# Optimization experiments

Hardware: AMD Instinct MI355X
Metric: run time of the kernel (lower is better)

## Reference

```python
import jax, jax.numpy as jnp
import numpy as np

EPS = 1e-6  # RMSNorm eps


def rms_norm(x, w):
    var = jnp.mean(jnp.square(x), axis=-1, keepdims=True)
    return x * jax.lax.rsqrt(var + EPS) * w


def setup_inputs() -> dict:
    B, N, D, L = 16, 4096, 512, 64
    key = jax.random.key(0)
    ks = jax.random.split(key, 12)
    query = jax.random.normal(ks[0], (B, D), jnp.float32)
    tokens = jax.random.normal(ks[1], (B, N, D), jnp.float32)
    padding_mask = jax.random.bernoulli(ks[2], 0.3, (B, N))  # True = padded
    latents = jax.random.normal(ks[3], (L, D), jnp.float32) * 0.02
    s = D ** -0.5
    Wq = jax.random.uniform(ks[4], (D, D), jnp.float32, -s, s)
    bq = jax.random.uniform(ks[5], (D,), jnp.float32, -s, s)
    Wk = jax.random.uniform(ks[6], (D, D), jnp.float32, -s, s)
    bk = jax.random.uniform(ks[7], (D,), jnp.float32, -s, s)
    Wv = jax.random.uniform(ks[8], (D, D), jnp.float32, -s, s)
    bv = jax.random.uniform(ks[9], (D,), jnp.float32, -s, s)
    norm_w = jnp.ones((D,), jnp.float32)
    return {"query": query, "tokens": tokens, "padding_mask": padding_mask,
            "latents": latents, "Wq": Wq, "bq": bq, "Wk": Wk, "bk": bk,
            "Wv": Wv, "bv": bv, "norm_w": norm_w}


def reference(query, tokens, padding_mask, latents, Wq, bq, Wk, bk, Wv, bv, norm_w):
    D = query.shape[-1]
    L = latents.shape[0]
    score_scale = float(D) ** -0.5

    valid = (~padding_mask).astype(tokens.dtype)[..., None]          # [B,N,1]
    masked_tokens = tokens * valid                                    # [B,N,D]

    latent_query = latents[None] + (query @ Wq + bq)[:, None, :]      # [B,L,D]
    keys = masked_tokens @ Wk + bk                                    # [B,N,D]
    values = (masked_tokens @ Wv + bv) * valid                        # [B,N,D]

    scores = jnp.einsum('bld,bnd->bln', latent_query, keys) * score_scale
    all_padded = jnp.all(padding_mask, axis=1, keepdims=True)         # [B,1]
    # safe key padding mask: if a row is entirely padded, unmask it to keep softmax finite
    safe_mask = (padding_mask & ~all_padded)[:, None, :]              # [B,1,N]
    scores = jnp.where(safe_mask, jnp.finfo(scores.dtype).min, scores)
    weights = jax.nn.softmax(scores.astype(jnp.float32), axis=-1).astype(values.dtype)

    out = jnp.einsum('bln,bnd->bld', weights, values)                 # [B,L,D]
    out = rms_norm(out, norm_w)
    out = out * (~all_padded).astype(out.dtype)[..., None]
    latent_mask = jnp.broadcast_to(all_padded, (all_padded.shape[0], L))
    return out, latent_mask
```

## Files before the change

kernel.cpp:

```cpp
#include <hip/hip_runtime.h>
#include <hip/hip_bf16.h>
#include <math.h>

#define BB 16
#define NN_ 4096
#define DD 512
#define LL 64
#define SCALE 0.044194173824159216f
#define RMS_EPS 1e-6f
#define MASKVAL -3.0e38f
#define PSZ (BB * LL * DD)
#define ZCH 16

using bf16x8 = __attribute__((ext_vector_type(8))) short;
using f32x4  = __attribute__((ext_vector_type(4))) float;

__device__ __forceinline__ unsigned short f2bf(float x) {
    return __bfloat16_as_ushort(__float2bfloat16(x));
}

__global__ __launch_bounds__(256) void k_qproj(const float* __restrict__ query, const float* __restrict__ Wq,
                                               const float* __restrict__ bq, float* __restrict__ qproj) {
    const int b = blockIdx.y;
    const int dl = threadIdx.x & 63;
    const int d = (blockIdx.x << 6) + dl;
    const int wv = threadIdx.x >> 6;
    __shared__ float q[DD];
    __shared__ float red[4][64];
    for (int e = threadIdx.x; e < DD; e += 256) q[e] = query[b * DD + e];
    __syncthreads();
    float acc = 0.f;
    #pragma unroll 8
    for (int i = 0; i < 128; ++i) {
        const int e = (wv << 7) + i;
        acc += q[e] * Wq[(size_t)e * DD + d];
    }
    red[wv][dl] = acc;
    __syncthreads();
    if (threadIdx.x < 64) {
        const int dd = (blockIdx.x << 6) + threadIdx.x;
        qproj[(size_t)b * DD + dd] = red[0][threadIdx.x] + red[1][threadIdx.x] +
                                     red[2][threadIdx.x] + red[3][threadIdx.x] + bq[dd];
    }
}

__global__ __launch_bounds__(256) void k_lkqk(const float* __restrict__ latents, const float* __restrict__ qproj,
                                              const float* __restrict__ Wk, const float* __restrict__ bk,
                                              float* __restrict__ Lk, float* __restrict__ Qk,
                                              float* __restrict__ sbL, float* __restrict__ sbQ) {
    const int r = blockIdx.y;
    const int e0 = blockIdx.x << 6;
    const int tid = threadIdx.x;
    __shared__ float row[DD];
    const float* src = (r < LL) ? (latents + (size_t)r * DD) : (qproj + (size_t)(r - LL) * DD);
    for (int dd = tid; dd < DD; dd += 256) row[dd] = src[dd];
    __syncthreads();
    const int e = e0 + (tid >> 2);
    const int part = tid & 3;
    const float4* w4 = (const float4*)(Wk + (size_t)e * DD);
    const float4* r4 = (const float4*)row;
    float acc = 0.f;
    #pragma unroll 8
    for (int j = 0; j < 32; ++j) {
        const int d4 = part + (j << 2);
        const float4 w = w4[d4], rr = r4[d4];
        acc += w.x * rr.x + w.y * rr.y + w.z * rr.z + w.w * rr.w;
    }
    acc += __shfl_xor(acc, 1);
    acc += __shfl_xor(acc, 2);
    if (part == 0) {
        if (r < LL) Lk[(size_t)r * DD + e] = acc;
        else        Qk[(size_t)(r - LL) * DD + e] = acc;
    }
    if (blockIdx.x == 0 && tid < 64) {
        float p = 0.f;
        #pragma unroll
        for (int dd = tid; dd < DD; dd += 64) p += bk[dd] * row[dd];
        #pragma unroll
        for (int off = 32; off > 0; off >>= 1) p += __shfl_xor(p, off);
        if (tid == 0) { if (r < LL) sbL[r] = p; else sbQ[r - LL] = p; }
    }
}

__global__ __launch_bounds__(512, 2) void k_flash(const float* __restrict__ tokens,
                                                  const float* __restrict__ Lk, const float* __restrict__ Qk,
                                                  const float* __restrict__ sbL, const float* __restrict__ sbQ,
                                                  const int* __restrict__ pmask,
                                                  float* __restrict__ part,
                                                  float* __restrict__ mz, float* __restrict__ sz) {
    const int z = blockIdx.x, b = blockIdx.y;
    const int tid = threadIdx.x;
    const int lane = tid & 63, w = tid >> 6;
    const int r16 = lane & 15, kl = lane >> 4;

    __shared__ unsigned short sB[64][72];
    __shared__ int sTdn[512][36];
    __shared__ unsigned short sP[64][72];
    __shared__ float sS[64][68];
    __shared__ float smem_m[64], smem_s[64], smem_rr[64], smem_ps[64];

    const int lq = (w & 3) << 4;
    const int nq = (w >> 2) << 5;
    bf16x8 afLQ[16];
    {
        const int l = lq + r16;
        #pragma unroll
        for (int f = 0; f < 16; ++f) {
            const int kb = (f << 5) + (kl << 3);
            const float4 a0 = *(const float4*)&Lk[(size_t)l * DD + kb];
            const float4 a1 = *(const float4*)&Lk[(size_t)l * DD + kb + 4];
            const float4 q0 = *(const float4*)&Qk[(size_t)b * DD + kb];
            const float4 q1 = *(const float4*)&Qk[(size_t)b * DD + kb + 4];
            bf16x8 v;
            v[0] = (short)f2bf(a0.x + q0.x); v[1] = (short)f2bf(a0.y + q0.y);
            v[2] = (short)f2bf(a0.z + q0.z); v[3] = (short)f2bf(a0.w + q0.w);
            v[4] = (short)f2bf(a1.x + q1.x); v[5] = (short)f2bf(a1.y + q1.y);
            v[6] = (short)f2bf(a1.z + q1.z); v[7] = (short)f2bf(a1.w + q1.w);
            afLQ[f] = v;
        }
    }

    f32x4 acc[4][4];
    #pragma unroll
    for (int m = 0; m < 4; ++m)
        #pragma unroll
        for (int ef = 0; ef < 4; ++ef)
            acc[m][ef] = (f32x4){0.f, 0.f, 0.f, 0.f};

    if (tid < 64) { smem_m[tid] = MASKVAL; smem_s[tid] = 0.f; }
    __syncthreads();

    const float sq = sbQ[b];
    const int n2 = tid >> 4;
    const int d4 = (tid & 15) << 2;

    for (int t4 = 0; t4 < 4; ++t4) {
        const int n0 = (z << 8) + (t4 << 6);
        f32x4 accS[2];
        accS[0] = (f32x4){0.f, 0.f, 0.f, 0.f};
        accS[1] = (f32x4){0.f, 0.f, 0.f, 0.f};

        float4 ra, rc;
        {
            const float* p0 = &tokens[(size_t)((b << 12) + n0 + (n2 << 1)) * DD + d4];
            ra = *(const float4*)p0; rc = *(const float4*)(p0 + DD);
        }
        #pragma unroll
        for (int s8 = 0; s8 < 8; ++s8) {
            const int d0 = s8 << 6;
            {
                ushort4 oa, oc;
                oa.x = f2bf(ra.x); oa.y = f2bf(ra.y); oa.z = f2bf(ra.z); oa.w = f2bf(ra.w);
                oc.x = f2bf(rc.x); oc.y = f2bf(rc.y); oc.z = f2bf(rc.z); oc.w = f2bf(rc.w);
                *(ushort4*)&sB[(n2 << 1)][d4] = oa;
                *(ushort4*)&sB[(n2 << 1) + 1][d4] = oc;
                const float* ap = (const float*)&ra;
                const float* cp = (const float*)&rc;
                #pragma unroll
                for (int j = 0; j < 4; ++j) {
                    const int drow = d0 + d4 + j;
                    const int phys = n2 ^ (((drow >> 2) & 7) << 2);
                    sTdn[drow][phys] = (int)((unsigned)f2bf(ap[j]) | ((unsigned)f2bf(cp[j]) << 16));
                }
            }
            __syncthreads();
            if (s8 < 7) {
                const float* p1 = &tokens[(size_t)((b << 12) + n0 + (n2 << 1)) * DD + ((s8 + 1) << 6) + d4];
                ra = *(const float4*)p1; rc = *(const float4*)(p1 + DD);
            }
            #pragma unroll
            for (int kk2 = 0; kk2 < 2; ++kk2) {
                const int f = (s8 << 1) + kk2;
                #pragma unroll
                for (int nf = 0; nf < 2; ++nf) {
                    const bf16x8 bfr = *(const bf16x8*)&sB[nq + (nf << 4) + r16][(kk2 << 5) + (kl << 3)];
                    accS[nf] = __builtin_amdgcn_mfma_f32_16x16x32_bf16(afLQ[f], bfr, accS[nf], 0, 0, 0);
                }
            }
            __syncthreads();
        }

        #pragma unroll
        for (int nf = 0; nf < 2; ++nf) {
            const int ncol = nq + (nf << 4) + r16;
            const int pm = pmask[(size_t)b * NN_ + n0 + ncol];
            #pragma unroll
            for (int q = 0; q < 4; ++q) {
                const int l = lq + (kl << 2) + q;
                const float sval = (accS[nf][q] + sbL[l] + sq) * SCALE;
                sS[l][ncol] = pm ? MASKVAL : sval;
            }
        }
        __syncthreads();

        const int lrow = tid >> 3, j8 = (tid & 7) << 3;
        float4 v0 = *(const float4*)&sS[lrow][j8];
        float4 v1 = *(const float4*)&sS[lrow][j8 + 4];
        float tm = fmaxf(fmaxf(fmaxf(v0.x, v0.y), fmaxf(v0.z, v0.w)),
                         fmaxf(fmaxf(v1.x, v1.y), fmaxf(v1.z, v1.w)));
        tm = fmaxf(tm, __shfl_xor(tm, 1));
        tm = fmaxf(tm, __shfl_xor(tm, 2));
        tm = fmaxf(tm, __shfl_xor(tm, 4));
        float ex[8];
        ex[0] = __expf(v0.x - tm); ex[1] = __expf(v0.y - tm);
        ex[2] = __expf(v0.z - tm); ex[3] = __expf(v0.w - tm);
        ex[4] = __expf(v1.x - tm); ex[5] = __expf(v1.y - tm);
        ex[6] = __expf(v1.z - tm); ex[7] = __expf(v1.w - tm);
        float ts = ex[0] + ex[1] + ex[2] + ex[3] + ex[4] + ex[5] + ex[6] + ex[7];
        ts += __shfl_xor(ts, 1);
        ts += __shfl_xor(ts, 2);
        ts += __shfl_xor(ts, 4);
        if ((tid & 7) == 0) {
            const float mo = smem_m[lrow];
            const float mn = fmaxf(mo, tm);
            const float rrr = __expf(mo - mn);
            const float psc = __expf(tm - mn);
            smem_m[lrow] = mn;
            smem_s[lrow] = smem_s[lrow] * rrr + ts * psc;
            smem_rr[lrow] = rrr;
            smem_ps[lrow] = psc;
        }
        __syncthreads();

        {
            const float psc = smem_ps[lrow];
            bf16x8 pv;
            pv[0] = (short)f2bf(ex[0] * psc); pv[1] = (short)f2bf(ex[1] * psc);
            pv[2] = (short)f2bf(ex[2] * psc); pv[3] = (short)f2bf(ex[3] * psc);
            pv[4] = (short)f2bf(ex[4] * psc); pv[5] = (short)f2bf(ex[5] * psc);
            pv[6] = (short)f2bf(ex[6] * psc); pv[7] = (short)f2bf(ex[7] * psc);
            *(bf16x8*)&sP[lrow][j8] = pv;
        }
        #pragma unroll
        for (int m = 0; m < 4; ++m) {
            #pragma unroll
            for (int q = 0; q < 4; ++q) {
                const float rrr = smem_rr[(m << 4) + (kl << 2) + q];
                #pragma unroll
                for (int ef = 0; ef < 4; ++ef) acc[m][ef][q] *= rrr;
            }
        }
        __syncthreads();

        #pragma unroll
        for (int kk = 0; kk < 2; ++kk) {
            bf16x8 pa[4];
            #pragma unroll
            for (int m = 0; m < 4; ++m)
                pa[m] = *(const bf16x8*)&sP[(m << 4) + r16][(kk << 5) + (kl << 3)];
            #pragma unroll
            for (int ef = 0; ef < 4; ++ef) {
                const int e = (w << 6) + (ef << 4) + r16;
                const int g = (kk << 4) + (kl << 2);
                const int phys = g ^ (((e >> 2) & 7) << 2);
                const bf16x8 bv = *(const bf16x8*)&sTdn[e][phys];
                #pragma unroll
                for (int m = 0; m < 4; ++m)
                    acc[m][ef] = __builtin_amdgcn_mfma_f32_16x16x32_bf16(pa[m], bv, acc[m][ef], 0, 0, 0);
            }
        }
        __syncthreads();
    }

    #pragma unroll
    for (int m = 0; m < 4; ++m) {
        #pragma unroll
        for (int ef = 0; ef < 4; ++ef) {
            #pragma unroll
            for (int q = 0; q < 4; ++q) {
                const int l = (m << 4) + (kl << 2) + q;
                const int e = (w << 6) + (ef << 4) + r16;
                part[(size_t)((z << 10) + (b << 6) + l) * DD + e] = acc[m][ef][q];
            }
        }
    }
    if (tid < 64) {
        mz[(z << 10) + (b << 6) + tid] = smem_m[tid];
        sz[(z << 10) + (b << 6) + tid] = smem_s[tid];
    }
}

__global__ __launch_bounds__(256) void k_combine(const float* __restrict__ part,
                                                 const float* __restrict__ mz, const float* __restrict__ sz,
                                                 float* __restrict__ pacc, float* __restrict__ dmg) {
    const int row = blockIdx.x;
    const int t = threadIdx.x;
    float mv[ZCH];
    float mg = MASKVAL;
    #pragma unroll
    for (int zz = 0; zz < ZCH; ++zz) {
        mv[zz] = mz[(zz << 10) + row];
        mg = fmaxf(mg, mv[zz]);
    }
    float fz[ZCH];
    float den = 0.f;
    #pragma unroll
    for (int zz = 0; zz < ZCH; ++zz) {
        fz[zz] = __expf(mv[zz] - mg);
        den += sz[(zz << 10) + row] * fz[zz];
    }
    float a0 = 0.f, a1 = 0.f;
    #pragma unroll
    for (int zz = 0; zz < ZCH; ++zz) {
        const size_t base = (size_t)((zz << 10) + row) * DD;
        a0 += part[base + t] * fz[zz];
        a1 += part[base + t + 256] * fz[zz];
    }
    const float inv = 1.f / den;
    pacc[(size_t)row * DD + t] = a0 * inv;
    pacc[(size_t)row * DD + t + 256] = a1 * inv;
    if (t == 0) dmg[row] = mg;
}

__global__ __launch_bounds__(256) void k_proj(const float* __restrict__ pacc, const float* __restrict__ Wv,
                                              const float* __restrict__ bv, float* __restrict__ proj) {
    const int d0 = blockIdx.x * 64;
    const int r0 = blockIdx.y * 64;
    const int tid = threadIdx.x;
    const int rsub = (tid >> 4) << 2;
    const int dsub = (tid & 15) << 2;
    __shared__ float at[64][68];
    __shared__ float wv[64][68];
    float acc[4][4] = {{0.f, 0.f, 0.f, 0.f}};
    for (int kc = 0; kc < 8; ++kc) {
        const int k0 = kc * 64;
        for (int k = tid; k < 1024; k += 256) {
            const int rr = k >> 4, c4 = (k & 15) << 2;
            *(float4*)&at[rr][c4] = *(const float4*)&pacc[(size_t)(r0 + rr) * DD + k0 + c4];
            *(float4*)&wv[rr][c4] = *(const float4*)&Wv[(size_t)(k0 + rr) * DD + d0 + c4];
        }
        __syncthreads();
        #pragma unroll
        for (int n4 = 0; n4 < 16; ++n4) {
            float4 a4[4];
            #pragma unroll
            for (int i = 0; i < 4; ++i) a4[i] = *(const float4*)&at[rsub + i][n4 << 2];
            const float4 b0 = *(const float4*)&wv[(n4 << 2) + 0][dsub];
            const float4 b1 = *(const float4*)&wv[(n4 << 2) + 1][dsub];
            const float4 b2 = *(const float4*)&wv[(n4 << 2) + 2][dsub];
            const float4 b3 = *(const float4*)&wv[(n4 << 2) + 3][dsub];
            #pragma unroll
            for (int i = 0; i < 4; ++i) {
                const float4 av = a4[i];
                acc[i][0] += av.x * b0.x + av.y * b1.x + av.z * b2.x + av.w * b3.x;
                acc[i][1] += av.x * b0.y + av.y * b1.y + av.z * b2.y + av.w * b3.y;
                acc[i][2] += av.x * b0.z + av.y * b1.z + av.z * b2.z + av.w * b3.z;
                acc[i][3] += av.x * b0.w + av.y * b1.w + av.z * b2.w + av.w * b3.w;
            }
        }
        __syncthreads();
    }
    #pragma unroll
    for (int i = 0; i < 4; ++i) {
        const int d = d0 + dsub;
        float4 v;
        v.x = acc[i][0] + bv[d + 0];
        v.y = acc[i][1] + bv[d + 1];
        v.z = acc[i][2] + bv[d + 2];
        v.w = acc[i][3] + bv[d + 3];
        *(float4*)&proj[(size_t)(r0 + rsub + i) * DD + d] = v;
    }
}

__global__ __launch_bounds__(256) void k_rmsout(const float* __restrict__ proj, const float* __restrict__ norm_w,
                                                const float* __restrict__ dmg, float* __restrict__ out) {
    const int row = blockIdx.x;
    const int tid = threadIdx.x;
    __shared__ float red[256];
    const float* pr = proj + (size_t)row * DD;
    const float v0 = pr[tid], v1 = pr[tid + 256];
    red[tid] = v0 * v0 + v1 * v1;
    __syncthreads();
    for (int st = 128; st > 0; st >>= 1) {
        if (tid < st) red[tid] += red[tid + st];
        __syncthreads();
    }
    const float var = red[0] / (float)DD;
    const float r = 1.0f / sqrtf(var + RMS_EPS);
    const int ap = (dmg[row] < -1.0e38f) ? 1 : 0;
    const float msk = ap ? 0.f : 1.f;
    out[(size_t)row * DD + tid]       = v0 * r * norm_w[tid] * msk;
    out[(size_t)row * DD + tid + 256] = v1 * r * norm_w[tid + 256] * msk;
    if (tid == 0) out[(size_t)PSZ + row] = ap ? 1.f : 0.f;
}

extern "C" void kernel_launch(void* const* d_in, const int* in_sizes, int n_in,
                              void* d_out, int out_size, void* d_ws, size_t ws_size,
                              hipStream_t stream) {
    const float* query   = (const float*)d_in[0];
    const float* tokens  = (const float*)d_in[1];
    const int*   pmask   = (const int*)d_in[2];
    const float* latents = (const float*)d_in[3];
    const float* Wq = (const float*)d_in[4];
    const float* bq = (const float*)d_in[5];
    const float* Wk = (const float*)d_in[6];
    const float* bk = (const float*)d_in[7];
    const float* Wv = (const float*)d_in[8];
    const float* bv = (const float*)d_in[9];
    const float* nw = (const float*)d_in[10];

    float* ws = (float*)d_ws;
    float* dmg    = ws;
    float* mzv    = ws + 1024;
    float* szv    = ws + 17408;
    float* qproj  = ws + 33792;
    float* Lk     = ws + 41984;
    float* Qk     = ws + 74752;
    float* sbL    = ws + 82944;
    float* sbQ    = ws + 83008;
    float* part   = ws + 83072;
    float* pacc   = ws + 83072 + 8388608;
    float* proj   = ws + 83072 + 8388608 + 524288;
    float* out    = (float*)d_out;

    k_qproj<<<dim3(8, 16), 256, 0, stream>>>(query, Wq, bq, qproj);
    k_lkqk<<<dim3(8, 80), 256, 0, stream>>>(latents, qproj, Wk, bk, Lk, Qk, sbL, sbQ);
    k_flash<<<dim3(ZCH, 16), 512, 0, stream>>>(tokens, Lk, Qk, sbL, sbQ, pmask, part, mzv, szv);
    k_combine<<<1024, 256, 0, stream>>>(part, mzv, szv, pacc, dmg);
    k_proj<<<dim3(8, 16), 256, 0, stream>>>(pacc, Wv, bv, proj);
    k_rmsout<<<1024, 256, 0, stream>>>(proj, nw, dmg, out);
}
```

Measured before the change: 105.0 us.

## Shrink flash LDS footprint, double split-K chunks, store partials in fp16

The token split is doubled from 16 to 32 chunks, so each block handles 128 tokens, and the occupancy hint rises from 2 to 6 blocks per CU. LDS is cut by dropping the large transposed token tile; tokens are re-read from global per wave into a small per-wave swizzled tile for the PV matmul. Softmax now works on register scores with cross-wave max/sum reductions instead of an LDS score matrix. Partial outputs are stored in fp16 to halve combine traffic, at some cost in precision and extra global token reads.

```diff
diff --git a/kernel.cpp b/kernel.cpp
--- a/kernel.cpp
+++ b/kernel.cpp
@@ -10,7 +10,7 @@
 #define RMS_EPS 1e-6f
 #define MASKVAL -3.0e38f
 #define PSZ (BB * LL * DD)
-#define ZCH 16
+#define ZCH 32
 
 using bf16x8 = __attribute__((ext_vector_type(8))) short;
 using f32x4  = __attribute__((ext_vector_type(4))) float;
@@ -82,22 +82,22 @@
     }
 }
 
-__global__ __launch_bounds__(512, 2) void k_flash(const float* __restrict__ tokens,
+__global__ __launch_bounds__(512, 6) void k_flash(const float* __restrict__ tokens,
                                                   const float* __restrict__ Lk, const float* __restrict__ Qk,
                                                   const float* __restrict__ sbL, const float* __restrict__ sbQ,
                                                   const int* __restrict__ pmask,
-                                                  float* __restrict__ part,
+                                                  _Float16* __restrict__ part,
                                                   float* __restrict__ mz, float* __restrict__ sz) {
     const int z = blockIdx.x, b = blockIdx.y;
     const int tid = threadIdx.x;
     const int lane = tid & 63, w = tid >> 6;
     const int r16 = lane & 15, kl = lane >> 4;
 
-    __shared__ unsigned short sB[64][72];
-    __shared__ int sTdn[512][36];
+    __shared__ int sB[64][32];
     __shared__ unsigned short sP[64][72];
-    __shared__ float sS[64][68];
-    __shared__ float smem_m[64], smem_s[64], smem_rr[64], smem_ps[64];
+    __shared__ int sT[8][64][16];
+    __shared__ float s_mn[64], s_sum[64], s_rr[64];
+    __shared__ float s_pmax[2][64], s_psum[2][64];
 
     const int lq = (w & 3) << 4;
     const int nq = (w >> 2) << 5;
@@ -120,6 +120,11 @@
         }
     }
 
+    float sbl[4];
+    #pragma unroll
+    for (int q = 0; q < 4; ++q) sbl[q] = sbL[lq + (kl << 2) + q];
+    const float sq = sbQ[b];
+
     f32x4 acc[4][4];
     #pragma unroll
     for (int m = 0; m < 4; ++m)
@@ -127,15 +132,17 @@
         for (int ef = 0; ef < 4; ++ef)
             acc[m][ef] = (f32x4){0.f, 0.f, 0.f, 0.f};
 
-    if (tid < 64) { smem_m[tid] = MASKVAL; smem_s[tid] = 0.f; }
+    if (tid < 64) { s_mn[tid] = MASKVAL; s_sum[tid] = 0.f; }
     __syncthreads();
 
-    const float sq = sbQ[b];
     const int n2 = tid >> 4;
-    const int d4 = (tid & 15) << 2;
-
-    for (int t4 = 0; t4 < 4; ++t4) {
-        const int n0 = (z << 8) + (t4 << 6);
+    const int l15 = tid & 15;
+    const int d4 = l15 << 2;
+    const int gB = (((n2 << 1) >> 2) & 7) << 2;
+    const int phB = ((l15 << 1) ^ gB);
+
+    for (int t = 0; t < 2; ++t) {
+        const int n0 = (z << 7) + (t << 6);
         f32x4 accS[2];
         accS[0] = (f32x4){0.f, 0.f, 0.f, 0.f};
         accS[1] = (f32x4){0.f, 0.f, 0.f, 0.f};
@@ -147,21 +154,14 @@
         }
         #pragma unroll
         for (int s8 = 0; s8 < 8; ++s8) {
-            const int d0 = s8 << 6;
             {
-                ushort4 oa, oc;
-                oa.x = f2bf(ra.x); oa.y = f2bf(ra.y); oa.z = f2bf(ra.z); oa.w = f2bf(ra.w);
-                oc.x = f2bf(rc.x); oc.y = f2bf(rc.y); oc.z = f2bf(rc.z); oc.w = f2bf(rc.w);
-                *(ushort4*)&sB[(n2 << 1)][d4] = oa;
-                *(ushort4*)&sB[(n2 << 1) + 1][d4] = oc;
-                const float* ap = (const float*)&ra;
-                const float* cp = (const float*)&rc;
-                #pragma unroll
-                for (int j = 0; j < 4; ++j) {
-                    const int drow = d0 + d4 + j;
-                    const int phys = n2 ^ (((drow >> 2) & 7) << 2);
-                    sTdn[drow][phys] = (int)((unsigned)f2bf(ap[j]) | ((unsigned)f2bf(cp[j]) << 16));
-                }
+                int2 wa, wc;
+                wa.x = (int)((unsigned)f2bf(ra.x) | ((unsigned)f2bf(ra.y) << 16));
+                wa.y = (int)((unsigned)f2bf(ra.z) | ((unsigned)f2bf(ra.w) << 16));
+                wc.x = (int)((unsigned)f2bf(rc.x) | ((unsigned)f2bf(rc.y) << 16));
+                wc.y = (int)((unsigned)f2bf(rc.z) | ((unsigned)f2bf(rc.w) << 16));
+                *(int2*)&sB[(n2 << 1)][phB] = wa;
+                *(int2*)&sB[(n2 << 1) + 1][phB] = wc;
             }
             __syncthreads();
             if (s8 < 7) {
@@ -173,87 +173,106 @@
                 const int f = (s8 << 1) + kk2;
                 #pragma unroll
                 for (int nf = 0; nf < 2; ++nf) {
-                    const bf16x8 bfr = *(const bf16x8*)&sB[nq + (nf << 4) + r16][(kk2 << 5) + (kl << 3)];
+                    const int nr = nq + (nf << 4) + r16;
+                    const int wo = (kk2 << 4) + (kl << 2);
+                    const int ph = wo ^ (((nr >> 2) & 7) << 2);
+                    const bf16x8 bfr = *(const bf16x8*)&sB[nr][ph];
                     accS[nf] = __builtin_amdgcn_mfma_f32_16x16x32_bf16(afLQ[f], bfr, accS[nf], 0, 0, 0);
                 }
             }
             __syncthreads();
         }
 
+        float sv[2][4];
         #pragma unroll
         for (int nf = 0; nf < 2; ++nf) {
             const int ncol = nq + (nf << 4) + r16;
             const int pm = pmask[(size_t)b * NN_ + n0 + ncol];
             #pragma unroll
             for (int q = 0; q < 4; ++q) {
-                const int l = lq + (kl << 2) + q;
-                const float sval = (accS[nf][q] + sbL[l] + sq) * SCALE;
-                sS[l][ncol] = pm ? MASKVAL : sval;
-            }
-        }
-        __syncthreads();
-
-        const int lrow = tid >> 3, j8 = (tid & 7) << 3;
-        float4 v0 = *(const float4*)&sS[lrow][j8];
-        float4 v1 = *(const float4*)&sS[lrow][j8 + 4];
-        float tm = fmaxf(fmaxf(fmaxf(v0.x, v0.y), fmaxf(v0.z, v0.w)),
-                         fmaxf(fmaxf(v1.x, v1.y), fmaxf(v1.z, v1.w)));
-        tm = fmaxf(tm, __shfl_xor(tm, 1));
-        tm = fmaxf(tm, __shfl_xor(tm, 2));
-        tm = fmaxf(tm, __shfl_xor(tm, 4));
-        float ex[8];
-        ex[0] = __expf(v0.x - tm); ex[1] = __expf(v0.y - tm);
-        ex[2] = __expf(v0.z - tm); ex[3] = __expf(v0.w - tm);
-        ex[4] = __expf(v1.x - tm); ex[5] = __expf(v1.y - tm);
-        ex[6] = __expf(v1.z - tm); ex[7] = __expf(v1.w - tm);
-        float ts = ex[0] + ex[1] + ex[2] + ex[3] + ex[4] + ex[5] + ex[6] + ex[7];
-        ts += __shfl_xor(ts, 1);
-        ts += __shfl_xor(ts, 2);
-        ts += __shfl_xor(ts, 4);
-        if ((tid & 7) == 0) {
-            const float mo = smem_m[lrow];
-            const float mn = fmaxf(mo, tm);
-            const float rrr = __expf(mo - mn);
-            const float psc = __expf(tm - mn);
-            smem_m[lrow] = mn;
-            smem_s[lrow] = smem_s[lrow] * rrr + ts * psc;
-            smem_rr[lrow] = rrr;
-            smem_ps[lrow] = psc;
-        }
-        __syncthreads();
-
-        {
-            const float psc = smem_ps[lrow];
-            bf16x8 pv;
-            pv[0] = (short)f2bf(ex[0] * psc); pv[1] = (short)f2bf(ex[1] * psc);
-            pv[2] = (short)f2bf(ex[2] * psc); pv[3] = (short)f2bf(ex[3] * psc);
-            pv[4] = (short)f2bf(ex[4] * psc); pv[5] = (short)f2bf(ex[5] * psc);
-            pv[6] = (short)f2bf(ex[6] * psc); pv[7] = (short)f2bf(ex[7] * psc);
-            *(bf16x8*)&sP[lrow][j8] = pv;
+                const float sval = (accS[nf][q] + sbl[q] + sq) * SCALE;
+                sv[nf][q] = pm ? MASKVAL : sval;
+            }
+        }
+        float tm[4];
+        #pragma unroll
+        for (int q = 0; q < 4; ++q) tm[q] = fmaxf(sv[0][q], sv[1][q]);
+        #pragma unroll
+        for (int off = 1; off <= 8; off <<= 1)
+            #pragma unroll
+            for (int q = 0; q < 4; ++q) tm[q] = fmaxf(tm[q], __shfl_xor(tm[q], off));
+        if (r16 == 0) {
+            #pragma unroll
+            for (int q = 0; q < 4; ++q) s_pmax[w >> 2][lq + (kl << 2) + q] = tm[q];
+        }
+        __syncthreads();
+        if (tid < 64) {
+            const float tmx = fmaxf(s_pmax[0][tid], s_pmax[1][tid]);
+            const float mo = s_mn[tid];
+            const float mn = fmaxf(mo, tmx);
+            s_rr[tid] = __expf(mo - mn);
+            s_mn[tid] = mn;
+        }
+        __syncthreads();
+        float mnq[4];
+        #pragma unroll
+        for (int q = 0; q < 4; ++q) mnq[q] = s_mn[lq + (kl << 2) + q];
+        float ps[4] = {0.f, 0.f, 0.f, 0.f};
+        #pragma unroll
+        for (int nf = 0; nf < 2; ++nf) {
+            const int ncol = nq + (nf << 4) + r16;
+            #pragma unroll
+            for (int q = 0; q < 4; ++q) {
+                const float p = __expf(sv[nf][q] - mnq[q]);
+                ps[q] += p;
+                sP[lq + (kl << 2) + q][ncol] = f2bf(p);
+            }
+        }
+        #pragma unroll
+        for (int off = 1; off <= 8; off <<= 1)
+            #pragma unroll
+            for (int q = 0; q < 4; ++q) ps[q] += __shfl_xor(ps[q], off);
+        if (r16 == 0) {
+            #pragma unroll
+            for (int q = 0; q < 4; ++q) s_psum[w >> 2][lq + (kl << 2) + q] = ps[q];
         }
         #pragma unroll
         for (int m = 0; m < 4; ++m) {
             #pragma unroll
             for (int q = 0; q < 4; ++q) {
-                const float rrr = smem_rr[(m << 4) + (kl << 2) + q];
+                const float rrr = s_rr[(m << 4) + (kl << 2) + q];
                 #pragma unroll
                 for (int ef = 0; ef < 4; ++ef) acc[m][ef][q] *= rrr;
             }
         }
         __syncthreads();
-
+        if (tid < 64) s_sum[tid] = s_sum[tid] * s_rr[tid] + s_psum[0][tid] + s_psum[1][tid];
+
+        const int sw = (lane >> 1) & 3;
+        const size_t tokbase = (size_t)((b << 12) + n0) * DD + (w << 6) + lane;
         #pragma unroll
         for (int kk = 0; kk < 2; ++kk) {
+            #pragma unroll
+            for (int q4 = 0; q4 < 4; ++q4) {
+                int wv0[4];
+                #pragma unroll
+                for (int jj = 0; jj < 4; ++jj) {
+                    const int nn = (kk << 5) + (q4 << 3) + (jj << 1);
+                    const float v0 = tokens[tokbase + (size_t)nn * DD];
+                    const float v1 = tokens[tokbase + (size_t)(nn + 1) * DD];
+                    wv0[jj] = (int)((unsigned)f2bf(v0) | ((unsigned)f2bf(v1) << 16));
+                }
+                *(int4*)&sT[w][lane][(q4 ^ sw) << 2] = make_int4(wv0[0], wv0[1], wv0[2], wv0[3]);
+            }
             bf16x8 pa[4];
             #pragma unroll
             for (int m = 0; m < 4; ++m)
                 pa[m] = *(const bf16x8*)&sP[(m << 4) + r16][(kk << 5) + (kl << 3)];
+            const int se = (r16 >> 1) & 3;
             #pragma unroll
             for (int ef = 0; ef < 4; ++ef) {
-                const int e = (w << 6) + (ef << 4) + r16;
-                const int g = (kk << 4) + (kl << 2);
-                const int phys = g ^ (((e >> 2) & 7) << 2);
-                const bf16x8 bv = *(const bf16x8*)&sTdn[e][phys];
+                const int er = (ef << 4) + r16;
+                const bf16x8 bv = *(const bf16x8*)&sT[w][er][(kl ^ se) << 2];
                 #pragma unroll
                 for (int m = 0; m < 4; ++m)
                     acc[m][ef] = __builtin_amdgcn_mfma_f32_16x16x32_bf16(pa[m], bv, acc[m][ef], 0, 0, 0);
@@ -270,41 +289,41 @@
             for (int q = 0; q < 4; ++q) {
                 const int l = (m << 4) + (kl << 2) + q;
                 const int e = (w << 6) + (ef << 4) + r16;
-                part[(size_t)((z << 10) + (b << 6) + l) * DD + e] = acc[m][ef][q];
+                part[(size_t)((z << 10) + (b << 6) + l) * DD + e] = (_Float16)acc[m][ef][q];
             }
         }
     }
     if (tid < 64) {
-        mz[(z << 10) + (b << 6) + tid] = smem_m[tid];
-        sz[(z << 10) + (b << 6) + tid] = smem_s[tid];
-    }
-}
-
-__global__ __launch_bounds__(256) void k_combine(const float* __restrict__ part,
+        mz[(z << 10) + (b << 6) + tid] = s_mn[tid];
+        sz[(z << 10) + (b << 6) + tid] = s_sum[tid];
+    }
+}
+
+__global__ __launch_bounds__(256) void k_combine(const _Float16* __restrict__ part,
                                                  const float* __restrict__ mz, const float* __restrict__ sz,
                                                  float* __restrict__ pacc, float* __restrict__ dmg) {
     const int row = blockIdx.x;
     const int t = threadIdx.x;
+    float mg = MASKVAL;
     float mv[ZCH];
-    float mg = MASKVAL;
     #pragma unroll
     for (int zz = 0; zz < ZCH; ++zz) {
         mv[zz] = mz[(zz << 10) + row];
         mg = fmaxf(mg, mv[zz]);
     }
+    float den = 0.f;
     float fz[ZCH];
-    float den = 0.f;
     #pragma unroll
     for (int zz = 0; zz < ZCH; ++zz) {
         fz[zz] = __expf(mv[zz] - mg);
         den += sz[(zz << 10) + row] * fz[zz];
     }
     float a0 = 0.f, a1 = 0.f;
-    #pragma unroll
+    #pragma unroll 8
     for (int zz = 0; zz < ZCH; ++zz) {
         const size_t base = (size_t)((zz << 10) + row) * DD;
-        a0 += part[base + t] * fz[zz];
-        a1 += part[base + t + 256] * fz[zz];
+        a0 += (float)part[base + t] * fz[zz];
+        a1 += (float)part[base + t + 256] * fz[zz];
     }
     const float inv = 1.f / den;
     pacc[(size_t)row * DD + t] = a0 * inv;
@@ -402,15 +421,15 @@
     float* ws = (float*)d_ws;
     float* dmg    = ws;
     float* mzv    = ws + 1024;
-    float* szv    = ws + 17408;
-    float* qproj  = ws + 33792;
-    float* Lk     = ws + 41984;
-    float* Qk     = ws + 74752;
-    float* sbL    = ws + 82944;
-    float* sbQ    = ws + 83008;
-    float* part   = ws + 83072;
-    float* pacc   = ws + 83072 + 8388608;
-    float* proj   = ws + 83072 + 8388608 + 524288;
+    float* szv    = ws + 33792;
+    float* qproj  = ws + 66560;
+    float* Lk     = ws + 74752;
+    float* Qk     = ws + 107520;
+    float* sbL    = ws + 115712;
+    float* sbQ    = ws + 115776;
+    _Float16* part = (_Float16*)(ws + 115968);
+    float* pacc   = ws + 115968 + 8388608;
+    float* proj   = ws + 115968 + 8388608 + 524288;
     float* out    = (float*)d_out;
 
     k_qproj<<<dim3(8, 16), 256, 0, stream>>>(query, Wq, bq, qproj);
```

After: 376.2 us. +258.2%, slower.
